# Performance work log

Measured on AMD Instinct MI355X. Metric: run time of the kernel, lower is better.

## Reference

```python
import jax, jax.numpy as jnp
import numpy as np

OFFSETS = jnp.array([[0., 0.], [1., 0.], [0., 1.], [1., 1.]], dtype=jnp.float32)  # 4x2 corner offsets


def gather_feat(feat, ind):
    # feat: [B, C, H, W], ind: [B, K] flat indices into H*W -> [B, K, C]
    B, C = feat.shape[0], feat.shape[1]
    f = feat.reshape(B, C, -1).transpose(0, 2, 1)  # [B, HW, C]
    return jnp.take_along_axis(f, ind[:, :, None], axis=1)


def iou(BoxA, BoxB):
    # Box[..., 0]=h, [...,1]=o_y, [...,2]=o_x ; broadcasts over leading dims
    hA, yA, xA = BoxA[..., 0], BoxA[..., 1], BoxA[..., 2]
    hB, yB, xB = BoxB[..., 0], BoxB[..., 1], BoxB[..., 2]
    areaA = hA * hA * 0.41
    areaB = hB * hB * 0.41
    y_min_max = jnp.maximum(yA - hA / 2, yB - hB / 2)
    x_min_max = jnp.maximum(xA - 0.41 * hA / 2, xB - 0.41 * hB / 2)
    y_max_min = jnp.minimum(yA + hA / 2, yB + hB / 2)
    x_max_min = jnp.minimum(xA + 0.41 * hA / 2, xB + 0.41 * hB / 2)
    I = jnp.clip(y_max_min - y_min_max, 0) * jnp.clip(x_max_min - x_min_max, 0)
    U = areaA + areaB - I
    return I / (U + 1e-6)


def setup_inputs() -> dict:
    key = jax.random.key(0)
    ks = jax.random.split(key, 9)
    B, N, M, HW = 64, 4096, 2048, 256 * 256
    return {
        'output_h': jax.random.normal(ks[0], (B, 1, 256, 256), jnp.float32),
        'output_off': jax.random.normal(ks[1], (B, 2, 256, 256), jnp.float32),
        'target_h': jax.random.normal(ks[2], (B, 1, 256, 256), jnp.float32),
        'target_off': jax.random.normal(ks[3], (B, 2, 256, 256), jnp.float32),
        'pre_off': jax.random.normal(ks[4], (B, M, 2), jnp.float32),
        'attract': jax.random.randint(ks[5], (B, N, 4), 0, HW, jnp.int32),
        'repel': jax.random.randint(ks[6], (B, M, 2, 4), 0, HW, jnp.int32),
        'mask_attract': jax.random.bernoulli(ks[7], 0.5, (B, N, 4)),
        'mask_repel': jax.random.bernoulli(ks[8], 0.5, (B, M, 1)),
    }


def reference(output_h, output_off, target_h, target_off, pre_off, attract, repel, mask_attract, mask_repel):
    B, N = attract.shape[0], attract.shape[1]
    M = repel.shape[1]

    # ---- attract branch ----
    attract_num = mask_attract.sum().astype(jnp.float32)
    attract_h = gather_feat(output_h, attract.reshape(B, -1)).reshape(B, N, 4, 1)
    attract_h_mean = attract_h.mean(2, keepdims=True)  # [B,N,1,1]
    attract_off = gather_feat(output_off, attract.reshape(B, -1)).reshape(B, N, 4, 2)
    attract_off = attract_off + OFFSETS.reshape(1, 1, 4, 2)
    attract_off_mean = attract_off.mean(2, keepdims=True)  # [B,N,1,2]
    attract_iou = iou(
        jnp.concatenate((jnp.exp(attract_h), attract_off), axis=-1),        # [B,N,4,3]
        jnp.concatenate((jnp.exp(attract_h_mean), attract_off_mean), axis=-1),  # [B,N,1,3]
    )  # [B,N,4]
    attract_loss = (1.0 - attract_iou) / (attract_num + 1e-4)
    attract_loss = jnp.where(mask_attract, attract_loss, 0.0).sum()

    # ---- repel branch ----
    repel_num = mask_repel.sum().astype(jnp.float32)
    repel_h = gather_feat(output_h, repel.reshape(B, -1)).reshape(B, M, 2, 4, 1)
    repel_h_mean = repel_h.mean(3, keepdims=True)  # [B,M,2,1,1]
    repel_off = gather_feat(output_off, repel.reshape(B, -1)).reshape(B, M, 2, 4, 2)
    repel_off = repel_off + OFFSETS.reshape(1, 1, 1, 4, 2)
    repel_off_mean = repel_off.mean(3, keepdims=True)  # [B,M,2,1,2]
    repel_off_mean = repel_off_mean.at[:, :, 1].add(pre_off[:, :, None, :])
    box = jnp.concatenate((jnp.exp(repel_h_mean), repel_off_mean), axis=-1)  # [B,M,2,1,3]
    repel_iou = iou(box[:, :, 0], box[:, :, 1])  # [B,M,1]
    repel_loss = repel_iou / (repel_num + 1e-4)
    repel_loss = jnp.where(mask_repel, repel_loss, 0.0).sum()

    return attract_loss + repel_loss
```

## Files before the change

### kernel.cpp

```cpp
#include <hip/hip_runtime.h>
#include <stdint.h>

#define HW    65536
#define LOG_N 12
#define LOG_M 11
#define BLK_PER_BATCH 24

__device__ __forceinline__ float iou_f(float hA, float yA, float xA,
                                       float hB, float yB, float xB) {
    float areaA = hA * hA * 0.41f;
    float areaB = hB * hB * 0.41f;
    float ymin = fmaxf(yA - hA * 0.5f,   yB - hB * 0.5f);
    float xmin = fmaxf(xA - 0.205f * hA, xB - 0.205f * hB);
    float ymax = fminf(yA + hA * 0.5f,   yB + hB * 0.5f);
    float xmax = fminf(xA + 0.205f * hA, xB + 0.205f * hB);
    float I = fmaxf(ymax - ymin, 0.f) * fmaxf(xmax - xmin, 0.f);
    float U = areaA + areaB - I;
    return I / (U + 1e-6f);
}

__device__ __forceinline__ void reduce_and_commit(float lsum, float lcnt,
                                                  float* dsum, float* dcnt) {
    #pragma unroll
    for (int off = 32; off > 0; off >>= 1) {
        lsum += __shfl_down(lsum, off, 64);
        lcnt += __shfl_down(lcnt, off, 64);
    }
    __shared__ float s0[4], s1[4];
    int lane = threadIdx.x & 63;
    int wid  = threadIdx.x >> 6;
    if (lane == 0) { s0[wid] = lsum; s1[wid] = lcnt; }
    __syncthreads();
    if (threadIdx.x == 0) {
        atomicAdd(dsum, s0[0] + s0[1] + s0[2] + s0[3]);
        atomicAdd(dcnt, s1[0] + s1[1] + s1[2] + s1[3]);
    }
}

__global__ __launch_bounds__(256)
void fused_kernel(const float* __restrict__ oh,
                  const float* __restrict__ ooff,
                  const float* __restrict__ pre,
                  const int*   __restrict__ attr,
                  const int*   __restrict__ rep,
                  const uint8_t* __restrict__ ma,
                  const uint8_t* __restrict__ mr,
                  float* __restrict__ ws, int swizzle) {
    int bid = blockIdx.x;
    int b, z;
    if (swizzle) {
        int x  = bid & 7;
        int y  = bid >> 3;
        int lb = y / BLK_PER_BATCH;
        z  = y - lb * BLK_PER_BATCH;
        b  = x + (lb << 3);
    } else {
        b = bid / BLK_PER_BATCH;
        z = bid - b * BLK_PER_BATCH;
    }

    const float* hb  = oh   + (size_t)b * HW;
    const float* oyb = ooff + (size_t)b * 2 * HW;
    const float* oxb = oyb + HW;

    if (z < 16) {
        int t = (b << LOG_N) + (z << 8) + threadIdx.x;
        int4 idx = *reinterpret_cast<const int4*>(attr + (size_t)t * 4);
        uint32_t m4 = *reinterpret_cast<const uint32_t*>(ma + (size_t)t * 4);

        float h0 = hb[idx.x], h1 = hb[idx.y], h2 = hb[idx.z], h3 = hb[idx.w];
        float y0 = oyb[idx.x],       y1 = oyb[idx.y] + 1.f,
              y2 = oyb[idx.z],       y3 = oyb[idx.w] + 1.f;
        float x0 = oxb[idx.x],       x1 = oxb[idx.y],
              x2 = oxb[idx.z] + 1.f, x3 = oxb[idx.w] + 1.f;

        float hm = (h0 + h1 + h2 + h3) * 0.25f;
        float ym = (y0 + y1 + y2 + y3) * 0.25f;
        float xm = (x0 + x1 + x2 + x3) * 0.25f;
        float ehm = expf(hm);

        float i0 = iou_f(expf(h0), y0, x0, ehm, ym, xm);
        float i1 = iou_f(expf(h1), y1, x1, ehm, ym, xm);
        float i2 = iou_f(expf(h2), y2, x2, ehm, ym, xm);
        float i3 = iou_f(expf(h3), y3, x3, ehm, ym, xm);

        float lsum = 0.f, lcnt = 0.f;
        if (m4 & 0x000000ffu) { lsum += 1.f - i0; lcnt += 1.f; }
        if (m4 & 0x0000ff00u) { lsum += 1.f - i1; lcnt += 1.f; }
        if (m4 & 0x00ff0000u) { lsum += 1.f - i2; lcnt += 1.f; }
        if (m4 & 0xff000000u) { lsum += 1.f - i3; lcnt += 1.f; }
        reduce_and_commit(lsum, lcnt, &ws[0], &ws[1]);
    } else {
        int t = (b << LOG_M) + ((z - 16) << 8) + threadIdx.x;
        const int* ip = rep + (size_t)t * 8;
        int4 ia = *reinterpret_cast<const int4*>(ip);
        int4 ib = *reinterpret_cast<const int4*>(ip + 4);

        float hm0 = (hb[ia.x] + hb[ia.y] + hb[ia.z] + hb[ia.w]) * 0.25f;
        float ym0 = (oyb[ia.x] + oyb[ia.y] + oyb[ia.z] + oyb[ia.w]) * 0.25f + 0.5f;
        float xm0 = (oxb[ia.x] + oxb[ia.y] + oxb[ia.z] + oxb[ia.w]) * 0.25f + 0.5f;

        float hm1 = (hb[ib.x] + hb[ib.y] + hb[ib.z] + hb[ib.w]) * 0.25f;
        float ym1 = (oyb[ib.x] + oyb[ib.y] + oyb[ib.z] + oyb[ib.w]) * 0.25f + 0.5f
                    + pre[(size_t)t * 2 + 0];
        float xm1 = (oxb[ib.x] + oxb[ib.y] + oxb[ib.z] + oxb[ib.w]) * 0.25f + 0.5f
                    + pre[(size_t)t * 2 + 1];

        float v = iou_f(expf(hm0), ym0, xm0, expf(hm1), ym1, xm1);
        float lsum = 0.f, lcnt = 0.f;
        if (mr[t]) { lsum = v; lcnt = 1.f; }
        reduce_and_commit(lsum, lcnt, &ws[2], &ws[3]);
    }
}

__global__ void finalize_kernel(const float* __restrict__ ws, float* __restrict__ out) {
    if (threadIdx.x == 0 && blockIdx.x == 0) {
        float v = ws[0] / (ws[1] + 1e-4f) + ws[2] / (ws[3] + 1e-4f);
        uint32_t bits = __float_as_uint(v);
        uint32_t lsb  = (bits >> 16) & 1u;
        uint32_t b16  = (bits + 0x7fffu + lsb) >> 16;
        uint32_t outw = (bits & 0xffff0000u) | (b16 & 0xffffu);
        reinterpret_cast<uint32_t*>(out)[0] = outw;
    }
}

extern "C" void kernel_launch(void* const* d_in, const int* in_sizes, int n_in,
                              void* d_out, int out_size, void* d_ws, size_t ws_size,
                              hipStream_t stream) {
    const float*   oh   = (const float*)d_in[0];
    const float*   ooff = (const float*)d_in[1];
    const float*   pre  = (const float*)d_in[4];
    const int*     attr = (const int*)d_in[5];
    const int*     rep  = (const int*)d_in[6];
    const uint8_t* ma   = (const uint8_t*)d_in[7];
    const uint8_t* mr   = (const uint8_t*)d_in[8];
    float* out = (float*)d_out;
    float* ws  = (float*)d_ws;

    int B = in_sizes[0] / HW;
    int swizzle = (B % 8 == 0) ? 1 : 0;
    int grid = B * BLK_PER_BATCH;

    hipMemsetAsync(d_ws, 0, 4 * sizeof(float), stream);
    fused_kernel<<<grid, 256, 0, stream>>>(oh, ooff, pre, attr, rep, ma, mr, ws, swizzle);
    finalize_kernel<<<1, 64, 0, stream>>>(ws, out);
}
```

Measured before the change: 166.1 us.

## Repack h/offset channels into interleaved float4 before random gathers

Adds a pre-pass kernel that interleaves output_h, off_y and off_x into one float4 per pixel in workspace memory. The gather kernel then fetches a single 16-byte element per index instead of three scattered 4-byte loads from separate planes. The aim is to cut the number of random memory transactions. The cost is an extra streaming pass that reads about 50MB and writes about 67MB. It falls back to the old fused kernel when the workspace is too small.

```diff
diff --git a/kernel.cpp b/kernel.cpp
--- a/kernel.cpp
+++ b/kernel.cpp
@@ -34,6 +34,100 @@
     if (threadIdx.x == 0) {
         atomicAdd(dsum, s0[0] + s0[1] + s0[2] + s0[3]);
         atomicAdd(dcnt, s1[0] + s1[1] + s1[2] + s1[3]);
+    }
+}
+
+__global__ __launch_bounds__(256)
+void pack_kernel(const float* __restrict__ oh,
+                 const float* __restrict__ ooff,
+                 float4* __restrict__ pk, int total4 ) {
+    for (int i = blockIdx.x * blockDim.x + threadIdx.x; i < total4;
+         i += gridDim.x * blockDim.x) {
+        int pos = i << 2;
+        int b   = pos >> 16;
+        int hw  = pos & (HW - 1);
+        const float4 h4 = *reinterpret_cast<const float4*>(oh + (size_t)b * HW + hw);
+        const float* oyb = ooff + (size_t)b * 2 * HW;
+        const float4 y4 = *reinterpret_cast<const float4*>(oyb + hw);
+        const float4 x4 = *reinterpret_cast<const float4*>(oyb + HW + hw);
+        float4* o = pk + pos;
+        o[0] = make_float4(h4.x, y4.x, x4.x, 0.f);
+        o[1] = make_float4(h4.y, y4.y, x4.y, 0.f);
+        o[2] = make_float4(h4.z, y4.z, x4.z, 0.f);
+        o[3] = make_float4(h4.w, y4.w, x4.w, 0.f);
+    }
+}
+
+__global__ __launch_bounds__(256)
+void gather_kernel(const float4* __restrict__ pk,
+                   const float* __restrict__ pre,
+                   const int*   __restrict__ attr,
+                   const int*   __restrict__ rep,
+                   const uint8_t* __restrict__ ma,
+                   const uint8_t* __restrict__ mr,
+                   float* __restrict__ ws, int swizzle) {
+    int bid = blockIdx.x;
+    int b, z;
+    if (swizzle) {
+        int x  = bid & 7;
+        int y  = bid >> 3;
+        int lb = y / BLK_PER_BATCH;
+        z  = y - lb * BLK_PER_BATCH;
+        b  = x + (lb << 3);
+    } else {
+        b = bid / BLK_PER_BATCH;
+        z = bid - b * BLK_PER_BATCH;
+    }
+
+    const float4* base = pk + (size_t)b * HW;
+
+    if (z < 16) {
+        int t = (b << LOG_N) + (z << 8) + threadIdx.x;
+        int4 idx = *reinterpret_cast<const int4*>(attr + (size_t)t * 4);
+        uint32_t m4 = *reinterpret_cast<const uint32_t*>(ma + (size_t)t * 4);
+
+        float4 v0 = base[idx.x], v1 = base[idx.y], v2 = base[idx.z], v3 = base[idx.w];
+        float h0 = v0.x, h1 = v1.x, h2 = v2.x, h3 = v3.x;
+        float y0 = v0.y,       y1 = v1.y + 1.f, y2 = v2.y,       y3 = v3.y + 1.f;
+        float x0 = v0.z,       x1 = v1.z,       x2 = v2.z + 1.f, x3 = v3.z + 1.f;
+
+        float hm = (h0 + h1 + h2 + h3) * 0.25f;
+        float ym = (y0 + y1 + y2 + y3) * 0.25f;
+        float xm = (x0 + x1 + x2 + x3) * 0.25f;
+        float ehm = expf(hm);
+
+        float i0 = iou_f(expf(h0), y0, x0, ehm, ym, xm);
+        float i1 = iou_f(expf(h1), y1, x1, ehm, ym, xm);
+        float i2 = iou_f(expf(h2), y2, x2, ehm, ym, xm);
+        float i3 = iou_f(expf(h3), y3, x3, ehm, ym, xm);
+
+        float lsum = 0.f, lcnt = 0.f;
+        if (m4 & 0x000000ffu) { lsum += 1.f - i0; lcnt += 1.f; }
+        if (m4 & 0x0000ff00u) { lsum += 1.f - i1; lcnt += 1.f; }
+        if (m4 & 0x00ff0000u) { lsum += 1.f - i2; lcnt += 1.f; }
+        if (m4 & 0xff000000u) { lsum += 1.f - i3; lcnt += 1.f; }
+        reduce_and_commit(lsum, lcnt, &ws[0], &ws[1]);
+    } else {
+        int t = (b << LOG_M) + ((z - 16) << 8) + threadIdx.x;
+        const int* ip = rep + (size_t)t * 8;
+        int4 ia = *reinterpret_cast<const int4*>(ip);
+        int4 ib = *reinterpret_cast<const int4*>(ip + 4);
+
+        float4 a0 = base[ia.x], a1 = base[ia.y], a2 = base[ia.z], a3 = base[ia.w];
+        float4 b0 = base[ib.x], b1 = base[ib.y], b2 = base[ib.z], b3 = base[ib.w];
+
+        float hm0 = (a0.x + a1.x + a2.x + a3.x) * 0.25f;
+        float ym0 = (a0.y + a1.y + a2.y + a3.y) * 0.25f + 0.5f;
+        float xm0 = (a0.z + a1.z + a2.z + a3.z) * 0.25f + 0.5f;
+
+        float hm1 = (b0.x + b1.x + b2.x + b3.x) * 0.25f;
+        float ym1 = (b0.y + b1.y + b2.y + b3.y) * 0.25f + 0.5f + pre[(size_t)t * 2 + 0];
+        float xm1 = (b0.z + b1.z + b2.z + b3.z) * 0.25f + 0.5f + pre[(size_t)t * 2 + 1];
+
+        float v = iou_f(expf(hm0), ym0, xm0, expf(hm1), ym1, xm1);
+        float lsum = 0.f, lcnt = 0.f;
+        if (mr[t]) { lsum = v; lcnt = 1.f; }
+        reduce_and_commit(lsum, lcnt, &ws[2], &ws[3]);
     }
 }
 
@@ -58,7 +152,6 @@
         b = bid / BLK_PER_BATCH;
         z = bid - b * BLK_PER_BATCH;
     }
-
     const float* hb  = oh   + (size_t)b * HW;
     const float* oyb = ooff + (size_t)b * 2 * HW;
     const float* oxb = oyb + HW;
@@ -67,23 +160,19 @@
         int t = (b << LOG_N) + (z << 8) + threadIdx.x;
         int4 idx = *reinterpret_cast<const int4*>(attr + (size_t)t * 4);
         uint32_t m4 = *reinterpret_cast<const uint32_t*>(ma + (size_t)t * 4);
-
         float h0 = hb[idx.x], h1 = hb[idx.y], h2 = hb[idx.z], h3 = hb[idx.w];
         float y0 = oyb[idx.x],       y1 = oyb[idx.y] + 1.f,
               y2 = oyb[idx.z],       y3 = oyb[idx.w] + 1.f;
         float x0 = oxb[idx.x],       x1 = oxb[idx.y],
               x2 = oxb[idx.z] + 1.f, x3 = oxb[idx.w] + 1.f;
-
         float hm = (h0 + h1 + h2 + h3) * 0.25f;
         float ym = (y0 + y1 + y2 + y3) * 0.25f;
         float xm = (x0 + x1 + x2 + x3) * 0.25f;
         float ehm = expf(hm);
-
         float i0 = iou_f(expf(h0), y0, x0, ehm, ym, xm);
         float i1 = iou_f(expf(h1), y1, x1, ehm, ym, xm);
         float i2 = iou_f(expf(h2), y2, x2, ehm, ym, xm);
         float i3 = iou_f(expf(h3), y3, x3, ehm, ym, xm);
-
         float lsum = 0.f, lcnt = 0.f;
         if (m4 & 0x000000ffu) { lsum += 1.f - i0; lcnt += 1.f; }
         if (m4 & 0x0000ff00u) { lsum += 1.f - i1; lcnt += 1.f; }
@@ -95,17 +184,14 @@
         const int* ip = rep + (size_t)t * 8;
         int4 ia = *reinterpret_cast<const int4*>(ip);
         int4 ib = *reinterpret_cast<const int4*>(ip + 4);
-
         float hm0 = (hb[ia.x] + hb[ia.y] + hb[ia.z] + hb[ia.w]) * 0.25f;
         float ym0 = (oyb[ia.x] + oyb[ia.y] + oyb[ia.z] + oyb[ia.w]) * 0.25f + 0.5f;
         float xm0 = (oxb[ia.x] + oxb[ia.y] + oxb[ia.z] + oxb[ia.w]) * 0.25f + 0.5f;
-
         float hm1 = (hb[ib.x] + hb[ib.y] + hb[ib.z] + hb[ib.w]) * 0.25f;
         float ym1 = (oyb[ib.x] + oyb[ib.y] + oyb[ib.z] + oyb[ib.w]) * 0.25f + 0.5f
                     + pre[(size_t)t * 2 + 0];
         float xm1 = (oxb[ib.x] + oxb[ib.y] + oxb[ib.z] + oxb[ib.w]) * 0.25f + 0.5f
                     + pre[(size_t)t * 2 + 1];
-
         float v = iou_f(expf(hm0), ym0, xm0, expf(hm1), ym1, xm1);
         float lsum = 0.f, lcnt = 0.f;
         if (mr[t]) { lsum = v; lcnt = 1.f; }
@@ -141,7 +227,17 @@
     int swizzle = (B % 8 == 0) ? 1 : 0;
     int grid = B * BLK_PER_BATCH;
 
+    size_t pack_bytes = (size_t)B * HW * sizeof(float4);
+    size_t needed = 256 + pack_bytes;
+
     hipMemsetAsync(d_ws, 0, 4 * sizeof(float), stream);
-    fused_kernel<<<grid, 256, 0, stream>>>(oh, ooff, pre, attr, rep, ma, mr, ws, swizzle);
+    if (ws_size >= needed) {
+        float4* pk = reinterpret_cast<float4*>((char*)d_ws + 256);
+        int total4 = (B * HW) >> 2;
+        pack_kernel<<<4096, 256, 0, stream>>>(oh, ooff, pk, total4);
+        gather_kernel<<<grid, 256, 0, stream>>>(pk, pre, attr, rep, ma, mr, ws, swizzle);
+    } else {
+        fused_kernel<<<grid, 256, 0, stream>>>(oh, ooff, pre, attr, rep, ma, mr, ws, swizzle);
+    }
     finalize_kernel<<<1, 64, 0, stream>>>(ws, out);
 }
```

After: 197.1 us. 1.19x slower.
